# Kernel optimization log

Hardware: AMD Instinct MI355X
Metric: run time of the kernel (lower is better)

## Reference

```python
import jax, jax.numpy as jnp
import numpy as np

NUM_HEADS = 12

def setup_inputs() -> dict:
    key = jax.random.key(0)
    k1, k2, k3 = jax.random.split(key, 3)
    B, N, C = 8, 2048, 768
    x = jax.random.normal(k1, (B, N, C), dtype=jnp.float32)
    w_qkv = jax.random.normal(k2, (3 * C, C), dtype=jnp.float32) * (C ** -0.5)
    w_proj = jax.random.normal(k3, (C, C), dtype=jnp.float32) * (C ** -0.5)
    b_proj = jnp.zeros((C,), dtype=jnp.float32)
    return {"x": x, "w_qkv": w_qkv, "w_proj": w_proj, "b_proj": b_proj}

def reference(x, w_qkv, w_proj, b_proj):
    B, N, C = x.shape
    H = NUM_HEADS
    D = C // H
    scale = D ** -0.5
    # qkv: [B,N,3C] -> [3,B,H,N,D]
    qkv = (x @ w_qkv.T).reshape(B, N, 3, H, D).transpose(2, 0, 3, 1, 4)
    q, k, v = qkv[0], qkv[1], qkv[2]
    attn = jnp.einsum('bhnd,bhmd->bhnm', q, k) * scale  # [B,H,N,N]
    attn = jax.nn.softmax(attn, axis=-1)
    out = jnp.einsum('bhnm,bhmd->bhnd', attn, v)  # [B,H,N,D]
    out = out.transpose(0, 2, 1, 3).reshape(B, N, C)
    return out @ w_proj.T + b_proj
```

## Files before the change

kernel.cpp:

```cpp
#include <hip/hip_runtime.h>

typedef __bf16 bf16;
typedef __attribute__((ext_vector_type(8))) __bf16 bf16x8;
typedef __attribute__((ext_vector_type(4))) __bf16 bf16x4;
typedef __attribute__((ext_vector_type(4))) float f32x4;

#define NBATCH 8
#define NHEAD  12
#define SEQ    2048
#define DH     64
#define CDIM   768
#define MROWS  (NBATCH*SEQ)
#define NQKV   (3*CDIM)

__device__ __forceinline__ f32x4 mfma16(bf16x8 a, bf16x8 b, f32x4 c) {
  return __builtin_amdgcn_mfma_f32_16x16x32_bf16(a, b, c, 0, 0, 0);
}

__device__ __forceinline__ void gload_lds16(const void* g, void* l) {
  __builtin_amdgcn_global_load_lds((const __attribute__((address_space(1))) void*)g,
                                   (__attribute__((address_space(3))) void*)l,
                                   16, 0, 0);
}

__device__ __forceinline__ unsigned cvt_pk_bf16(float lo, float hi) {
  unsigned r;
  asm("v_cvt_pk_bf16_f32 %0, %1, %2" : "=v"(r) : "v"(lo), "v"(hi));
  return r;
}

__device__ __forceinline__ float exp2_raw(float x) {
  float r;
  asm("v_exp_f32 %0, %1" : "=v"(r) : "v"(x));
  return r;
}

__global__ __launch_bounds__(256)
void cvt_all(const float* __restrict__ x, const float* __restrict__ wq,
             const float* __restrict__ wp, bf16* __restrict__ xd,
             bf16* __restrict__ wqd, bf16* __restrict__ wpd) {
  const int bid = blockIdx.x;
  const float* s;
  bf16* d;
  int i;
  if (bid < 6144)      { s = x;  d = xd;  i = bid * 256 + threadIdx.x; }
  else if (bid < 7008) { s = wq; d = wqd; i = (bid - 6144) * 256 + threadIdx.x; }
  else                 { s = wp; d = wpd; i = (bid - 7008) * 256 + threadIdx.x; }
  const float4* s4 = (const float4*)s;
  float4 a = s4[2*i], c = s4[2*i+1];
  bf16x8 o;
  o[0]=(bf16)a.x; o[1]=(bf16)a.y; o[2]=(bf16)a.z; o[3]=(bf16)a.w;
  o[4]=(bf16)c.x; o[5]=(bf16)c.y; o[6]=(bf16)c.z; o[7]=(bf16)c.w;
  *(bf16x8*)(d + (size_t)i*8) = o;
}

template <int OUT_F32>
__global__ __launch_bounds__(256, 3)
void gemm_bt(const bf16* __restrict__ A, const bf16* __restrict__ Bm,
             void* __restrict__ Cout, const float* __restrict__ bias,
             int M, int Nn, int K) {
  __shared__ bf16 As[2][128*32];
  __shared__ bf16 Bs[2][128*32];
  const int tid = threadIdx.x, wid = tid >> 6, lane = tid & 63;
  const int g = lane >> 4, ln = lane & 15;
  const int ntn = Nn >> 7;
  const int gsz = 32 * ntn;
  const int grp = blockIdx.x / gsz;
  const int rem = blockIdx.x - grp * gsz;
  const int tm = grp * 32 + (rem & 31);
  const int tn = rem >> 5;
  const int m0 = tm << 7, n0 = tn << 7;
  const int wr = wid >> 1, wc = wid & 1;

  const int srow = lane >> 2;
  const int sslot = lane & 3;
  const int c0 = wid * 2, c1 = wid * 2 + 1;
  const int row0 = c0 * 16 + srow, row1 = c1 * 16 + srow;
  const int sw0 = (sslot ^ (row0 & 3)) << 3;
  const int sw1 = (sslot ^ (row1 & 3)) << 3;
  const bf16* a0 = A + (size_t)(m0 + row0) * K + sw0;
  const bf16* a1 = A + (size_t)(m0 + row1) * K + sw1;
  const bf16* b0 = Bm + (size_t)(n0 + row0) * K + sw0;
  const bf16* b1 = Bm + (size_t)(n0 + row1) * K + sw1;

  f32x4 acc[4][4] = {};
  const int nkt = K >> 5;

#define GSTAGE(BUF) do {                                          \
    gload_lds16(a0, &As[BUF][c0 * 512]);                          \
    gload_lds16(a1, &As[BUF][c1 * 512]);                          \
    gload_lds16(b0, &Bs[BUF][c0 * 512]);                          \
    gload_lds16(b1, &Bs[BUF][c1 * 512]);                          \
    a0 += 32; a1 += 32; b0 += 32; b1 += 32;                       \
  } while (0)

  GSTAGE(0);
  GSTAGE(1);

  for (int kt = 0; kt < nkt; ++kt) {
    if (kt < nkt - 1) asm volatile("s_waitcnt vmcnt(4)" ::: "memory");
    else              asm volatile("s_waitcnt vmcnt(0)" ::: "memory");
    __builtin_amdgcn_s_barrier();
    __builtin_amdgcn_sched_barrier(0);

    const bf16* AsB = &As[kt & 1][0];
    const bf16* BsB = &Bs[kt & 1][0];
    bf16x8 aF[4], bF[4];
    #pragma unroll
    for (int m = 0; m < 4; ++m) {
      int row = wr * 64 + m * 16 + ln;
      aF[m] = *(const bf16x8*)&AsB[row * 32 + ((g ^ (row & 3)) << 3)];
    }
    #pragma unroll
    for (int n = 0; n < 4; ++n) {
      int row = wc * 64 + n * 16 + ln;
      bF[n] = *(const bf16x8*)&BsB[row * 32 + ((g ^ (row & 3)) << 3)];
    }
    #pragma unroll
    for (int m = 0; m < 4; ++m)
      #pragma unroll
      for (int n = 0; n < 4; ++n)
        acc[m][n] = mfma16(aF[m], bF[n], acc[m][n]);

    __builtin_amdgcn_sched_barrier(0);
    __builtin_amdgcn_s_barrier();
    if (kt + 2 < nkt) GSTAGE(kt & 1);
  }
#undef GSTAGE

  #pragma unroll
  for (int m = 0; m < 4; ++m) {
    int rowb = m0 + wr * 64 + m * 16 + g * 4;
    #pragma unroll
    for (int n = 0; n < 4; ++n) {
      int col = n0 + wc * 64 + n * 16 + ln;
      float bv = OUT_F32 ? bias[col] : 0.f;
      #pragma unroll
      for (int r = 0; r < 4; ++r) {
        if (OUT_F32)
          ((float*)Cout)[(size_t)(rowb + r) * Nn + col] = acc[m][n][r] + bv;
        else
          ((bf16*)Cout)[(size_t)(rowb + r) * Nn + col] = (bf16)acc[m][n][r];
      }
    }
  }
}

__global__ __launch_bounds__(256)
void split_v(const bf16* __restrict__ qkv, bf16* __restrict__ Vt) {
  __shared__ bf16 vlds[64 * 72];
  const int nt = blockIdx.x, bh = blockIdx.y;
  const int b = bh / NHEAD, h = bh % NHEAD;
  const int tid = threadIdx.x;
  const int nl = tid >> 2, quad = tid & 3;

  const bf16* s = qkv + ((size_t)(b * SEQ + nt * 64 + nl)) * NQKV + 2 * CDIM + h * DH + quad * 16;
  *(bf16x8*)&vlds[nl * 72 + quad * 16] = *(const bf16x8*)s;
  *(bf16x8*)&vlds[nl * 72 + quad * 16 + 8] = *(const bf16x8*)(s + 8);
  __syncthreads();
  const int dl = tid >> 2;
  bf16x8 w0, w1;
  #pragma unroll
  for (int j = 0; j < 8; ++j) {
    w0[j] = vlds[(quad * 16 + j) * 72 + dl];
    w1[j] = vlds[(quad * 16 + 8 + j) * 72 + dl];
  }
  bf16* d = Vt + ((size_t)bh * DH + dl) * SEQ + nt * 64 + quad * 16;
  *(bf16x8*)d = w0;
  *(bf16x8*)(d + 8) = w1;
}

__global__ __launch_bounds__(512, 4)
void attn_fwd12(const bf16* __restrict__ qkv, const bf16* __restrict__ Vt,
                bf16* __restrict__ Oa) {
  __shared__ bf16 Ks[2][4096];
  __shared__ bf16 Vs[2][4096];
  const int tid = threadIdx.x, wid = tid >> 6, lane = tid & 63;
  const int g = lane >> 4, ln = lane & 15;
  const int qt = blockIdx.x, bh = blockIdx.y;
  const int b = bh / NHEAD, h = bh % NHEAD;

  const bf16* QrowA = qkv + ((size_t)b * SEQ + qt * 256 + wid * 32 + ln) * NQKV + h * DH;
  const bf16* QrowB = QrowA + (size_t)16 * NQKV;
  const bf16x8 qA0 = *(const bf16x8*)(QrowA + g * 8);
  const bf16x8 qA1 = *(const bf16x8*)(QrowA + 32 + g * 8);
  const bf16x8 qB0 = *(const bf16x8*)(QrowB + g * 8);
  const bf16x8 qB1 = *(const bf16x8*)(QrowB + 32 + g * 8);

  const int sr = lane >> 3, sl = lane & 7;
  const int pr = wid * 8 + sr;
  const int sw = (sl ^ (pr & 7)) << 3;
  const int keyK = ((pr >> 5) & 1) * 32 + ((pr >> 4) & 1) * 4 + ((pr >> 2) & 3) * 8 + (pr & 3);
  const bf16* kp = qkv + ((size_t)b * SEQ + keyK) * NQKV + CDIM + h * DH + sw;
  const bf16* vp = Vt + ((size_t)bh * DH + pr) * SEQ + sw;
  const int lofs = wid * 512;
  const size_t KADV = (size_t)64 * NQKV;

  const int e7 = ln & 7;
  const int off0 = ln * 64 + ((g ^ e7) << 3);
  const int off1 = ln * 64 + (((4 | g) ^ e7) << 3);

  const bf16 one = (bf16)1.0f;
  const bf16x8 onesF = {one, one, one, one, one, one, one, one};

  f32x4 oA[4] = {}, oB[4] = {};
  f32x4 laccA = {0.f, 0.f, 0.f, 0.f}, laccB = {0.f, 0.f, 0.f, 0.f};
  float mA = -3.0e38f, mB = -3.0e38f;
  const float SC = 0.125f * 1.44269504088896f;

  gload_lds16(kp, &Ks[0][lofs]);
  gload_lds16(vp, &Vs[0][lofs]);
  kp += KADV; vp += 64;
  gload_lds16(kp, &Ks[1][lofs]);
  gload_lds16(vp, &Vs[1][lofs]);
  kp += KADV; vp += 64;

  const int NT = SEQ / 64;
  for (int t = 0; t < NT; ++t) {
    if (t == NT - 1) asm volatile("s_waitcnt vmcnt(0)" ::: "memory");
    else             asm volatile("s_waitcnt vmcnt(2)" ::: "memory");
    __builtin_amdgcn_s_barrier();
    __builtin_amdgcn_sched_barrier(0);

    const bf16* KsB = &Ks[t & 1][0];
    const bf16* VsB = &Vs[t & 1][0];

    f32x4 sA[4] = {}, sB[4] = {};
    #pragma unroll
    for (int nt = 0; nt < 4; ++nt) {
      bf16x8 kF0 = *(const bf16x8*)(KsB + off0 + nt * 1024);
      bf16x8 kF1 = *(const bf16x8*)(KsB + off1 + nt * 1024);
      sA[nt] = mfma16(kF0, qA0, sA[nt]);
      sA[nt] = mfma16(kF1, qA1, sA[nt]);
      sB[nt] = mfma16(kF0, qB0, sB[nt]);
      sB[nt] = mfma16(kF1, qB1, sB[nt]);
    }

    float a0 = fmaxf(fmaxf(sA[0][0], sA[0][1]), fmaxf(sA[0][2], sA[0][3]));
    float a1 = fmaxf(fmaxf(sA[1][0], sA[1][1]), fmaxf(sA[1][2], sA[1][3]));
    float a2 = fmaxf(fmaxf(sA[2][0], sA[2][1]), fmaxf(sA[2][2], sA[2][3]));
    float a3 = fmaxf(fmaxf(sA[3][0], sA[3][1]), fmaxf(sA[3][2], sA[3][3]));
    float rA = fmaxf(fmaxf(a0, a1), fmaxf(a2, a3));
    rA = fmaxf(rA, __shfl_xor(rA, 16, 64));
    rA = fmaxf(rA, __shfl_xor(rA, 32, 64));
    float b0 = fmaxf(fmaxf(sB[0][0], sB[0][1]), fmaxf(sB[0][2], sB[0][3]));
    float b1 = fmaxf(fmaxf(sB[1][0], sB[1][1]), fmaxf(sB[1][2], sB[1][3]));
    float b2 = fmaxf(fmaxf(sB[2][0], sB[2][1]), fmaxf(sB[2][2], sB[2][3]));
    float b3 = fmaxf(fmaxf(sB[3][0], sB[3][1]), fmaxf(sB[3][2], sB[3][3]));
    float rB = fmaxf(fmaxf(b0, b1), fmaxf(b2, b3));
    rB = fmaxf(rB, __shfl_xor(rB, 16, 64));
    rB = fmaxf(rB, __shfl_xor(rB, 32, 64));
    const float rsA = rA * SC, rsB = rB * SC;

    if (__any(rsA > mA + 8.0f || rsB > mB + 8.0f)) {
      float nmA = fmaxf(mA, rsA), nmB = fmaxf(mB, rsB);
      float alA = exp2_raw(mA - nmA), alB = exp2_raw(mB - nmB);
      mA = nmA; mB = nmB;
      float alrA[4], alrB[4];
      #pragma unroll
      for (int r = 0; r < 4; ++r) {
        alrA[r] = __shfl(alA, g * 4 + r, 64);
        alrB[r] = __shfl(alB, g * 4 + r, 64);
      }
      #pragma unroll
      for (int dt = 0; dt < 4; ++dt)
        #pragma unroll
        for (int r = 0; r < 4; ++r) { oA[dt][r] *= alrA[r]; oB[dt][r] *= alrB[r]; }
      #pragma unroll
      for (int r = 0; r < 4; ++r) { laccA[r] *= alrA[r]; laccB[r] *= alrB[r]; }
    }

    bf16x8 pA[2], pB[2];
    #pragma unroll
    for (int kk = 0; kk < 2; ++kk) {
      union { bf16x8 v; unsigned u[4]; } w;
      w.u[0] = cvt_pk_bf16(exp2_raw(fmaf(sA[2*kk][0], SC, -mA)),
                           exp2_raw(fmaf(sA[2*kk][1], SC, -mA)));
      w.u[1] = cvt_pk_bf16(exp2_raw(fmaf(sA[2*kk][2], SC, -mA)),
                           exp2_raw(fmaf(sA[2*kk][3], SC, -mA)));
      w.u[2] = cvt_pk_bf16(exp2_raw(fmaf(sA[2*kk+1][0], SC, -mA)),
                           exp2_raw(fmaf(sA[2*kk+1][1], SC, -mA)));
      w.u[3] = cvt_pk_bf16(exp2_raw(fmaf(sA[2*kk+1][2], SC, -mA)),
                           exp2_raw(fmaf(sA[2*kk+1][3], SC, -mA)));
      pA[kk] = w.v;
      w.u[0] = cvt_pk_bf16(exp2_raw(fmaf(sB[2*kk][0], SC, -mB)),
                           exp2_raw(fmaf(sB[2*kk][1], SC, -mB)));
      w.u[1] = cvt_pk_bf16(exp2_raw(fmaf(sB[2*kk][2], SC, -mB)),
                           exp2_raw(fmaf(sB[2*kk][3], SC, -mB)));
      w.u[2] = cvt_pk_bf16(exp2_raw(fmaf(sB[2*kk+1][0], SC, -mB)),
                           exp2_raw(fmaf(sB[2*kk+1][1], SC, -mB)));
      w.u[3] = cvt_pk_bf16(exp2_raw(fmaf(sB[2*kk+1][2], SC, -mB)),
                           exp2_raw(fmaf(sB[2*kk+1][3], SC, -mB)));
      pB[kk] = w.v;
    }

    #pragma unroll
    for (int kk = 0; kk < 2; ++kk) {
      laccA = mfma16(pA[kk], onesF, laccA);
      laccB = mfma16(pB[kk], onesF, laccB);
      const int voff = kk ? off1 : off0;
      #pragma unroll
      for (int dt = 0; dt < 4; ++dt) {
        bf16x8 vF = *(const bf16x8*)(VsB + voff + dt * 1024);
        oA[dt] = mfma16(pA[kk], vF, oA[dt]);
        oB[dt] = mfma16(pB[kk], vF, oB[dt]);
      }
    }

    __builtin_amdgcn_sched_barrier(0);
    __builtin_amdgcn_s_barrier();
    if (t + 2 < NT) {
      gload_lds16(kp, &Ks[t & 1][lofs]);
      gload_lds16(vp, &Vs[t & 1][lofs]);
      kp += KADV; vp += 64;
    }
  }

  float invA[4], invB[4];
  #pragma unroll
  for (int r = 0; r < 4; ++r) { invA[r] = 1.0f / laccA[r]; invB[r] = 1.0f / laccB[r]; }

  #pragma unroll
  for (int r = 0; r < 4; ++r) {
    bf16* OrA = Oa + ((size_t)b * SEQ + qt * 256 + wid * 32 + g * 4 + r) * CDIM + h * DH + ln;
    bf16* OrB = OrA + (size_t)16 * CDIM;
    #pragma unroll
    for (int dt = 0; dt < 4; ++dt) {
      OrA[dt * 16] = (bf16)(oA[dt][r] * invA[r]);
      OrB[dt * 16] = (bf16)(oB[dt][r] * invB[r]);
    }
  }
}

extern "C" void kernel_launch(void* const* d_in, const int* in_sizes, int n_in,
                              void* d_out, int out_size, void* d_ws, size_t ws_size,
                              hipStream_t stream) {
  const float* x      = (const float*)d_in[0];
  const float* w_qkv  = (const float*)d_in[1];
  const float* w_proj = (const float*)d_in[2];
  const float* b_proj = (const float*)d_in[3];

  char* ws = (char*)d_ws;
  bf16* x_bf    = (bf16*)(ws + 0);
  bf16* wqkv_bf = (bf16*)(ws + 25165824);
  bf16* wproj_bf= (bf16*)(ws + 28704768);
  bf16* qkv     = (bf16*)(ws + 29884416);
  bf16* attn_o  = (bf16*)(ws + 105381888);
  bf16* Vtb     = (bf16*)(ws + 130547712);

  cvt_all<<<dim3(7296), 256, 0, stream>>>(x, w_qkv, w_proj, x_bf, wqkv_bf, wproj_bf);

  gemm_bt<0><<<dim3((MROWS/128)*(NQKV/128)), 256, 0, stream>>>(
      x_bf, wqkv_bf, qkv, nullptr, MROWS, NQKV, CDIM);

  split_v<<<dim3(SEQ/64, NBATCH*NHEAD), 256, 0, stream>>>(qkv, Vtb);

  attn_fwd12<<<dim3(SEQ/256, NBATCH*NHEAD), 512, 0, stream>>>(qkv, Vtb, attn_o);

  gemm_bt<1><<<dim3((MROWS/128)*(CDIM/128)), 256, 0, stream>>>(
      attn_o, wproj_bf, (float*)d_out, b_proj, MROWS, CDIM, CDIM);
}
```

Baseline: 258.3 us.

## Use 256x256 tile triple-buffered GEMM with 512 threads for QKV projection

```diff
diff --git a/kernel.cpp b/kernel.cpp
--- a/kernel.cpp
+++ b/kernel.cpp
@@ -52,6 +52,110 @@
   o[0]=(bf16)a.x; o[1]=(bf16)a.y; o[2]=(bf16)a.z; o[3]=(bf16)a.w;
   o[4]=(bf16)c.x; o[5]=(bf16)c.y; o[6]=(bf16)c.z; o[7]=(bf16)c.w;
   *(bf16x8*)(d + (size_t)i*8) = o;
+}
+
+template <int OUT_F32>
+__global__ __launch_bounds__(512, 2)
+void gemm_bt2(const bf16* __restrict__ A, const bf16* __restrict__ Bm,
+              void* __restrict__ Cout, const float* __restrict__ bias,
+              int M, int Nn, int K) {
+  __shared__ bf16 As[3][8192];
+  __shared__ bf16 Bs[3][8192];
+  const int tid = threadIdx.x, wid = tid >> 6, lane = tid & 63;
+  const int g = lane >> 4, ln = lane & 15;
+  const int ntm = M >> 8;
+  const int tm = blockIdx.x % ntm;
+  const int tn = blockIdx.x / ntm;
+  const int m0 = tm << 8, n0 = tn << 8;
+  const int wr = wid >> 2, wc = wid & 3;
+
+  const int srow = tid >> 2;
+  const int sslot = tid & 3;
+  const int sw = ((sslot ^ (srow & 3)) << 3);
+  const bf16* a0 = A + (size_t)(m0 + srow) * K + sw;
+  const bf16* a1 = A + (size_t)(m0 + 128 + srow) * K + sw;
+  const bf16* b0 = Bm + (size_t)(n0 + srow) * K + sw;
+  const bf16* b1 = Bm + (size_t)(n0 + 128 + srow) * K + sw;
+  const int l0 = tid * 8, l1 = 4096 + tid * 8;
+
+  const int colsw = (g ^ (ln & 3)) << 3;
+  const int aBase = (wr * 128 + ln) * 32 + colsw;
+  const int bBase = (wc * 64 + ln) * 32 + colsw;
+
+  f32x4 acc[8][4] = {};
+  const int nkt = K >> 5;
+
+#define STA2(SB) do { gload_lds16(a0, &As[SB][l0]); gload_lds16(a1, &As[SB][l1]); a0 += 32; a1 += 32; } while (0)
+#define STB2(SB) do { gload_lds16(b0, &Bs[SB][l0]); gload_lds16(b1, &Bs[SB][l1]); b0 += 32; b1 += 32; } while (0)
+
+  STA2(0); STB2(0);
+  STA2(1); STB2(1);
+
+  int buf = 0;
+  for (int kt = 0; kt < nkt; ++kt) {
+    if (kt < nkt - 1) asm volatile("s_waitcnt vmcnt(4)" ::: "memory");
+    else              asm volatile("s_waitcnt vmcnt(0)" ::: "memory");
+    __builtin_amdgcn_s_barrier();
+    __builtin_amdgcn_sched_barrier(0);
+
+    const bf16* AsB = &As[buf][0];
+    const bf16* BsB = &Bs[buf][0];
+    int sbuf = buf + 2; if (sbuf >= 3) sbuf -= 3;
+
+    bf16x8 bF[4];
+    #pragma unroll
+    for (int n = 0; n < 4; ++n)
+      bF[n] = *(const bf16x8*)(BsB + bBase + n * 512);
+
+    if (kt + 2 < nkt) STA2(sbuf);
+
+    bf16x8 aF0[4];
+    #pragma unroll
+    for (int m = 0; m < 4; ++m)
+      aF0[m] = *(const bf16x8*)(AsB + aBase + m * 512);
+    __builtin_amdgcn_s_setprio(1);
+    #pragma unroll
+    for (int m = 0; m < 4; ++m)
+      #pragma unroll
+      for (int n = 0; n < 4; ++n)
+        acc[m][n] = mfma16(aF0[m], bF[n], acc[m][n]);
+    __builtin_amdgcn_s_setprio(0);
+
+    if (kt + 2 < nkt) STB2(sbuf);
+
+    bf16x8 aF1[4];
+    #pragma unroll
+    for (int m = 0; m < 4; ++m)
+      aF1[m] = *(const bf16x8*)(AsB + aBase + (4 + m) * 512);
+    __builtin_amdgcn_s_setprio(1);
+    #pragma unroll
+    for (int m = 0; m < 4; ++m)
+      #pragma unroll
+      for (int n = 0; n < 4; ++n)
+        acc[4 + m][n] = mfma16(aF1[m], bF[n], acc[4 + m][n]);
+    __builtin_amdgcn_s_setprio(0);
+
+    buf = (buf + 1 == 3) ? 0 : buf + 1;
+  }
+#undef STA2
+#undef STB2
+
+  #pragma unroll
+  for (int m = 0; m < 8; ++m) {
+    int rowb = m0 + wr * 128 + m * 16 + g * 4;
+    #pragma unroll
+    for (int n = 0; n < 4; ++n) {
+      int col = n0 + wc * 64 + n * 16 + ln;
+      float bv = OUT_F32 ? bias[col] : 0.f;
+      #pragma unroll
+      for (int r = 0; r < 4; ++r) {
+        if (OUT_F32)
+          ((float*)Cout)[(size_t)(rowb + r) * Nn + col] = acc[m][n][r] + bv;
+        else
+          ((bf16*)Cout)[(size_t)(rowb + r) * Nn + col] = (bf16)acc[m][n][r];
+      }
+    }
+  }
 }
 
 template <int OUT_F32>
@@ -350,7 +454,7 @@
 
   cvt_all<<<dim3(7296), 256, 0, stream>>>(x, w_qkv, w_proj, x_bf, wqkv_bf, wproj_bf);
 
-  gemm_bt<0><<<dim3((MROWS/128)*(NQKV/128)), 256, 0, stream>>>(
+  gemm_bt2<0><<<dim3((MROWS/256)*(NQKV/256)), 512, 0, stream>>>(
       x_bf, wqkv_bf, qkv, nullptr, MROWS, NQKV, CDIM);
 
   split_v<<<dim3(SEQ/64, NBATCH*NHEAD), 256, 0, stream>>>(qkv, Vtb);
```

New measurement: 267.1 us. +3.4%, slower.
